# Kernel tuning notes

Hardware: AMD Instinct MI355X
Metric: run time of the kernel (lower is better)

## Reference

```python
import jax, jax.numpy as jnp
import numpy as np

K_STEPS = 10
ALPHA = 0.1
N_NODES = 100000
N_EDGES = 3200000

def setup_inputs() -> dict:
    key = jax.random.key(0)
    ks = jax.random.split(key, 6)
    x = jax.random.normal(ks[0], (N_NODES, 512), dtype=jnp.float32)
    edge_index = jax.random.randint(ks[1], (2, N_EDGES), 0, N_NODES, dtype=jnp.int64)
    W1 = jax.random.normal(ks[2], (512, 128), dtype=jnp.float32) * (1.0 / np.sqrt(512))
    b1 = jnp.zeros((128,), dtype=jnp.float32)
    W2 = jax.random.normal(ks[3], (128, 64), dtype=jnp.float32) * (1.0 / np.sqrt(128))
    b2 = jnp.zeros((64,), dtype=jnp.float32)
    return {"x": x, "edge_index": edge_index, "W1": W1, "b1": b1, "W2": W2, "b2": b2}

def _appnp_propagate(h, edge_index, n_nodes):
    # gcn_norm with self-loops: A_hat = D^-1/2 (A + I) D^-1/2
    self_loops = jnp.arange(n_nodes, dtype=edge_index.dtype)
    row = jnp.concatenate([edge_index[0], self_loops])  # source
    col = jnp.concatenate([edge_index[1], self_loops])  # target
    ew = jnp.ones(row.shape[0], dtype=h.dtype)
    deg = jax.ops.segment_sum(ew, col, num_segments=n_nodes)
    dis = jnp.where(deg > 0, jax.lax.rsqrt(deg), 0.0)
    norm = dis[row] * dis[col]  # [E+N]
    out = h
    for _ in range(K_STEPS):
        msg = norm[:, None] * out[row]                       # gather [E+N, C]
        agg = jax.ops.segment_sum(msg, col, num_segments=n_nodes)  # scatter
        out = (1.0 - ALPHA) * agg + ALPHA * h
    return out

def reference(x, edge_index, W1, b1, W2, b2):
    # eval mode: dropout is identity
    h = jax.nn.relu(x @ W1 + b1)
    h = h @ W2 + b2
    out = _appnp_propagate(h, edge_index, x.shape[0])
    return jax.nn.log_softmax(out, axis=1)
```

## Files before the change

kernel.cpp:

```cpp
#include <hip/hip_runtime.h>
#include <hip/hip_bf16.h>

#define N_NODES 100000
#define N_EDGES 3200000
#define C_OUT 64
#define C_HID 128
#define C_IN 512

typedef unsigned short u16;
typedef unsigned int u32;
using short8 = __attribute__((ext_vector_type(8))) short;
using f32x4 = __attribute__((ext_vector_type(4))) float;

__device__ __forceinline__ u32 f2bf(float f) {
    u32 x = __float_as_uint(f);
    return (x + 0x7fffu + ((x >> 16) & 1u)) >> 16;
}
__device__ __forceinline__ float bf2f_lo(u32 u) { return __uint_as_float(u << 16); }
__device__ __forceinline__ float bf2f_hi(u32 u) { return __uint_as_float(u & 0xffff0000u); }

__global__ __launch_bounds__(256) void hist_kernel(const int* __restrict__ cols,
                                                   int* __restrict__ cnt) {
    int e = blockIdx.x * 256 + threadIdx.x;
    if (e < N_EDGES) atomicAdd(&cnt[cols[e]], 1);
}

__global__ __launch_bounds__(256) void dis_kernel(const int* __restrict__ cnt,
                                                  float* __restrict__ dis) {
    int i = blockIdx.x * 256 + threadIdx.x;
    if (i < N_NODES) dis[i] = rsqrtf((float)(cnt[i] + 1));
}

__global__ __launch_bounds__(256) void scanA(const int* __restrict__ cnt,
                                             int* __restrict__ offs,
                                             int* __restrict__ bsum, int n) {
    __shared__ int sh[256];
    int b = blockIdx.x, tid = threadIdx.x;
    int base = b * 1024;
    int v[4]; int s = 0;
#pragma unroll
    for (int i = 0; i < 4; i++) {
        int idx = base + tid * 4 + i;
        v[i] = (idx < n) ? cnt[idx] : 0;
        s += v[i];
    }
    sh[tid] = s;
    __syncthreads();
    for (int st = 1; st < 256; st <<= 1) {
        int a = (tid >= st) ? sh[tid - st] : 0;
        int t = sh[tid];
        __syncthreads();
        sh[tid] = t + a;
        __syncthreads();
    }
    int run = sh[tid] - s;
#pragma unroll
    for (int i = 0; i < 4; i++) {
        int idx = base + tid * 4 + i;
        run += v[i];
        if (idx < n) offs[idx + 1] = run;
    }
    if (tid == 255) bsum[b] = sh[255];
}

__global__ __launch_bounds__(256) void scanB(int* __restrict__ bsum, int nb) {
    __shared__ int sh[256];
    int tid = threadIdx.x;
    int v = (tid < nb) ? bsum[tid] : 0;
    sh[tid] = v;
    __syncthreads();
    for (int st = 1; st < 256; st <<= 1) {
        int a = (tid >= st) ? sh[tid - st] : 0;
        int t = sh[tid];
        __syncthreads();
        sh[tid] = t + a;
        __syncthreads();
    }
    if (tid < nb) bsum[tid] = sh[tid] - v;
}

__global__ __launch_bounds__(256) void scanC(int* __restrict__ offs,
                                             const int* __restrict__ bsum, int n) {
    int idx = blockIdx.x * 256 + threadIdx.x;
    if (idx < n) offs[idx + 1] += bsum[idx >> 10];
    if (idx == 0) offs[0] = 0;
}

__global__ __launch_bounds__(256) void fill_kernel(const int* __restrict__ rows,
                                                   const int* __restrict__ cols,
                                                   const float* __restrict__ dis,
                                                   const int* __restrict__ offs,
                                                   int* __restrict__ cursor,
                                                   int* __restrict__ csr_row,
                                                   float* __restrict__ csr_norm) {
    int e = blockIdx.x * 256 + threadIdx.x;
    if (e >= N_EDGES) return;
    int r = rows[e], c = cols[e];
    float w = dis[r] * dis[c];
    int p = atomicAdd(&cursor[c], 1);
    int idx = offs[c] + p;
    csr_row[idx] = r;
    csr_norm[idx] = w;
}

__global__ __launch_bounds__(256) void w1t_kernel(const float* __restrict__ W1,
                                                  u16* __restrict__ W1T) {
    int idx = blockIdx.x * 256 + threadIdx.x;
    int n = idx >> 9, k = idx & 511;
    W1T[idx] = (u16)f2bf(W1[k * C_HID + n]);
}

__global__ __launch_bounds__(256) void gemm1_mfma(const float* __restrict__ X,
                                                  const u16* __restrict__ W1T,
                                                  const float* __restrict__ B1,
                                                  float* __restrict__ H1) {
    __shared__ u16 xs[64][56];
    __shared__ u16 wsT[128][56];
    int tid = threadIdx.x;
    int w = tid >> 6, l = tid & 63;
    int row0 = blockIdx.x * 64;

    f32x4 acc[8];
#pragma unroll
    for (int j = 0; j < 8; j++) acc[j] = (f32x4){0.f, 0.f, 0.f, 0.f};

    const int sr = tid >> 2;
    const int skq = (tid & 3) * 8;
    const int wn = tid >> 1;
    const int wkh = (tid & 1) * 16;

    for (int kb = 0; kb < C_IN; kb += 32) {
        {
            int gr = row0 + sr;
            float4 v0 = {0, 0, 0, 0}, v1 = {0, 0, 0, 0};
            if (gr < N_NODES) {
                const float4* px =
                    reinterpret_cast<const float4*>(X + (size_t)gr * C_IN + kb + skq);
                v0 = px[0];
                v1 = px[1];
            }
            uint4 pk;
            pk.x = f2bf(v0.x) | (f2bf(v0.y) << 16);
            pk.y = f2bf(v0.z) | (f2bf(v0.w) << 16);
            pk.z = f2bf(v1.x) | (f2bf(v1.y) << 16);
            pk.w = f2bf(v1.z) | (f2bf(v1.w) << 16);
            *reinterpret_cast<uint4*>(&xs[sr][skq]) = pk;
        }
        {
            const uint4* pw =
                reinterpret_cast<const uint4*>(W1T + (size_t)wn * C_IN + kb + wkh);
            *reinterpret_cast<uint4*>(&wsT[wn][wkh]) = pw[0];
            *reinterpret_cast<uint4*>(&wsT[wn][wkh + 8]) = pw[1];
        }
        __syncthreads();
        int ar = w * 16 + (l & 15);
        int koff = (l >> 4) * 8;
        short8 a = *reinterpret_cast<const short8*>(&xs[ar][koff]);
#pragma unroll
        for (int j = 0; j < 8; j++) {
            short8 b = *reinterpret_cast<const short8*>(&wsT[j * 16 + (l & 15)][koff]);
            acc[j] = __builtin_amdgcn_mfma_f32_16x16x32_bf16(a, b, acc[j], 0, 0, 0);
        }
        __syncthreads();
    }
    int col_lo = l & 15;
    int rbase = row0 + w * 16 + (l >> 4) * 4;
#pragma unroll
    for (int j = 0; j < 8; j++) {
        int col = j * 16 + col_lo;
        float bias = B1[col];
#pragma unroll
        for (int rr = 0; rr < 4; rr++) {
            int grow = rbase + rr;
            if (grow < N_NODES) {
                float v = acc[j][rr] + bias;
                H1[(size_t)grow * C_HID + col] = v > 0.f ? v : 0.f;
            }
        }
    }
}

__global__ __launch_bounds__(256) void gemm2(const float* __restrict__ H1,
                                             const float* __restrict__ W2,
                                             const float* __restrict__ B2,
                                             float* __restrict__ H) {
    __shared__ float hs[64][132];
    __shared__ float ws[128][64];
    int tid = threadIdx.x;
    int tx = tid & 15, ty = tid >> 4;
    int row0 = blockIdx.x * 64;
#pragma unroll
    for (int l = 0; l < 8; l++) {
        int idx = tid + l * 256;
        int k = idx >> 4;
        int c4 = idx & 15;
        *reinterpret_cast<float4*>(&ws[k][c4 * 4]) =
            *reinterpret_cast<const float4*>(W2 + (size_t)k * C_OUT + c4 * 4);
    }
#pragma unroll
    for (int l = 0; l < 8; l++) {
        int idx = tid + l * 256;
        int r = idx >> 5;
        int k4 = idx & 31;
        int gr = row0 + r;
        float4 v = {0, 0, 0, 0};
        if (gr < N_NODES)
            v = *reinterpret_cast<const float4*>(H1 + (size_t)gr * C_HID + k4 * 4);
        hs[r][k4 * 4 + 0] = v.x;
        hs[r][k4 * 4 + 1] = v.y;
        hs[r][k4 * 4 + 2] = v.z;
        hs[r][k4 * 4 + 3] = v.w;
    }
    __syncthreads();
    float acc[4][4];
#pragma unroll
    for (int i = 0; i < 4; i++)
#pragma unroll
        for (int j = 0; j < 4; j++) acc[i][j] = 0.f;
#pragma unroll 4
    for (int k = 0; k < C_HID; k++) {
        float hv[4], wv[4];
#pragma unroll
        for (int i = 0; i < 4; i++) hv[i] = hs[ty * 4 + i][k];
#pragma unroll
        for (int j = 0; j < 4; j++) wv[j] = ws[k][tx * 4 + j];
#pragma unroll
        for (int i = 0; i < 4; i++)
#pragma unroll
            for (int j = 0; j < 4; j++) acc[i][j] += hv[i] * wv[j];
    }
#pragma unroll
    for (int i = 0; i < 4; i++) {
        int gr = row0 + ty * 4 + i;
        if (gr < N_NODES) {
#pragma unroll
            for (int j = 0; j < 4; j++) {
                int c = tx * 4 + j;
                H[(size_t)gr * C_OUT + c] = acc[i][j] + B2[c];
            }
        }
    }
}

__global__ __launch_bounds__(256) void conv_bf16(const float* __restrict__ h,
                                                 u16* __restrict__ hb) {
    int idx = blockIdx.x * 256 + threadIdx.x;
    if (idx < N_NODES * 16) {
        float4 v = reinterpret_cast<const float4*>(h)[idx];
        uint2 o;
        o.x = f2bf(v.x) | (f2bf(v.y) << 16);
        o.y = f2bf(v.z) | (f2bf(v.w) << 16);
        reinterpret_cast<uint2*>(hb)[idx] = o;
    }
}

__global__ __launch_bounds__(256) void prop_bf16(const u16* __restrict__ src,
                                                 const float* __restrict__ hsrc,
                                                 u16* __restrict__ dst,
                                                 const int* __restrict__ offs,
                                                 const int* __restrict__ csr_row,
                                                 const float* __restrict__ csr_norm,
                                                 const float* __restrict__ dis) {
    int wid = (blockIdx.x * 256 + threadIdx.x) >> 6;
    if (wid >= N_NODES) return;
    int lane = threadIdx.x & 63;
    int g = lane >> 4;
    int cq = lane & 15;
    int beg = offs[wid], end = offs[wid + 1];
    float a0 = 0.f, a1 = 0.f, a2 = 0.f, a3 = 0.f;
    for (int j = beg; j < end; j += 4) {
        int jj = j + g;
        int r = 0;
        float w = 0.f;
        if (jj < end) {
            r = csr_row[jj];
            w = csr_norm[jj];
        }
        uint2 v = *reinterpret_cast<const uint2*>(src + ((size_t)r << 6) + (cq << 2));
        a0 += w * bf2f_lo(v.x);
        a1 += w * bf2f_hi(v.x);
        a2 += w * bf2f_lo(v.y);
        a3 += w * bf2f_hi(v.y);
    }
    a0 += __shfl_xor(a0, 16); a0 += __shfl_xor(a0, 32);
    a1 += __shfl_xor(a1, 16); a1 += __shfl_xor(a1, 32);
    a2 += __shfl_xor(a2, 16); a2 += __shfl_xor(a2, 32);
    a3 += __shfl_xor(a3, 16); a3 += __shfl_xor(a3, 32);
    if (g == 0) {
        float d = dis[wid];
        float d2 = d * d;
        size_t base = ((size_t)wid << 6) + (cq << 2);
        uint2 sv = *reinterpret_cast<const uint2*>(src + base);
        const float4 hv = *reinterpret_cast<const float4*>(hsrc + base);
        float o0 = 0.9f * (a0 + d2 * bf2f_lo(sv.x)) + 0.1f * hv.x;
        float o1 = 0.9f * (a1 + d2 * bf2f_hi(sv.x)) + 0.1f * hv.y;
        float o2 = 0.9f * (a2 + d2 * bf2f_lo(sv.y)) + 0.1f * hv.z;
        float o3 = 0.9f * (a3 + d2 * bf2f_hi(sv.y)) + 0.1f * hv.w;
        uint2 ov;
        ov.x = f2bf(o0) | (f2bf(o1) << 16);
        ov.y = f2bf(o2) | (f2bf(o3) << 16);
        *reinterpret_cast<uint2*>(dst + base) = ov;
    }
}

__global__ __launch_bounds__(256) void logsm_kernel(const u16* __restrict__ src,
                                                    float* __restrict__ out) {
    int wid = (blockIdx.x * 256 + threadIdx.x) >> 6;
    if (wid >= N_NODES) return;
    int lane = threadIdx.x & 63;
    float v = __uint_as_float(((u32)src[((size_t)wid << 6) + lane]) << 16);
    float m = v;
#pragma unroll
    for (int s = 1; s < 64; s <<= 1) m = fmaxf(m, __shfl_xor(m, s));
    float e = __expf(v - m);
    float sum = e;
#pragma unroll
    for (int s = 1; s < 64; s <<= 1) sum += __shfl_xor(sum, s);
    out[((size_t)wid << 6) + lane] = (v - m) - __logf(sum);
}

extern "C" void kernel_launch(void* const* d_in, const int* in_sizes, int n_in,
                              void* d_out, int out_size, void* d_ws, size_t ws_size,
                              hipStream_t stream) {
    const float* x = (const float*)d_in[0];
    const int* ei = (const int*)d_in[1];
    const float* W1 = (const float*)d_in[2];
    const float* B1 = (const float*)d_in[3];
    const float* W2 = (const float*)d_in[4];
    const float* B2 = (const float*)d_in[5];
    float* out = (float*)d_out;

    const int* rows = ei;
    const int* cols = ei + N_EDGES;

    char* p = (char*)d_ws;
    float* h1 = (float*)p;
    p += (size_t)N_NODES * C_HID * 4;
    float* h = (float*)p;
    p += (size_t)N_NODES * C_OUT * 4;
    int* csr_row = (int*)p;  p += (size_t)N_EDGES * 4;
    float* csr_norm = (float*)p; p += (size_t)N_EDGES * 4;
    int* cnt = (int*)p;      p += (size_t)N_NODES * 4;
    int* offs = (int*)p;     p += (size_t)(N_NODES + 1) * 4;
    int* cursor = (int*)p;   p += (size_t)N_NODES * 4;
    float* dis = (float*)p;  p += (size_t)N_NODES * 4;
    int* bsum = (int*)p;     p += 256 * 4;

    u16* W1T = (u16*)cursor;

    u16* hb = (u16*)h1;
    u16* stA = hb + (size_t)N_NODES * C_OUT;
    u16* stB = stA + (size_t)N_NODES * C_OUT;

    hipMemsetAsync(cnt, 0, (size_t)N_NODES * 4, stream);
    hipMemsetAsync(cursor, 0, (size_t)N_NODES * 4, stream);

    const int egrid = (N_EDGES + 255) / 256;
    const int ngrid = (N_NODES + 255) / 256;
    const int nscan = (N_NODES + 1023) / 1024;

    hist_kernel<<<egrid, 256, 0, stream>>>(cols, cnt);
    dis_kernel<<<ngrid, 256, 0, stream>>>(cnt, dis);
    scanA<<<nscan, 256, 0, stream>>>(cnt, offs, bsum, N_NODES);
    scanB<<<1, 256, 0, stream>>>(bsum, nscan);
    scanC<<<ngrid, 256, 0, stream>>>(offs, bsum, N_NODES);
    fill_kernel<<<egrid, 256, 0, stream>>>(rows, cols, dis, offs, cursor, csr_row, csr_norm);

    w1t_kernel<<<256, 256, 0, stream>>>(W1, W1T);

    const int mgrid = (N_NODES + 63) / 64;
    gemm1_mfma<<<mgrid, 256, 0, stream>>>(x, W1T, B1, h1 );
    gemm2<<<mgrid, 256, 0, stream>>>(h1, W2, B2, h);
    conv_bf16<<<(N_NODES * 16 + 255) / 256, 256, 0, stream>>>(h, hb);

    const int pgrid = N_NODES / 4;
    const u16* src = hb;
    u16* dst = stA;
    for (int k = 0; k < 10; k++) {
        prop_bf16<<<pgrid, 256, 0, stream>>>(src, h, dst, offs, csr_row, csr_norm, dis);
        src = dst;
        dst = (dst == stA) ? stB : stA;
    }
    logsm_kernel<<<pgrid, 256, 0, stream>>>(src, out);
}
```

Measured before the change: 1.727 ms.

## Pack CSR as int2 and widen propagation gathers to 16-byte loads

Interleaves the CSR source index and edge weight into a single 8-byte array so each edge needs one load. The propagation kernel is restructured to use 8 lanes per 64-channel row with 16-byte gathers, and processes 16 edges per iteration with two independent gathers per lane. Nontemporal loads are used for streaming edge data. This aims to raise memory-level parallelism and cut load instruction count in the gather-bound propagation, at the cost of more padding work for nodes whose degree is not a multiple of 16 and more registers.

New measurement: 1.388 ms. 19.7% less time.

```diff
diff --git a/kernel.cpp b/kernel.cpp
--- a/kernel.cpp
+++ b/kernel.cpp
@@ -9,6 +9,7 @@
 
 typedef unsigned short u16;
 typedef unsigned int u32;
+typedef long long ll;
 using short8 = __attribute__((ext_vector_type(8))) short;
 using f32x4 = __attribute__((ext_vector_type(4))) float;
 
@@ -22,7 +23,7 @@
 __global__ __launch_bounds__(256) void hist_kernel(const int* __restrict__ cols,
                                                    int* __restrict__ cnt) {
     int e = blockIdx.x * 256 + threadIdx.x;
-    if (e < N_EDGES) atomicAdd(&cnt[cols[e]], 1);
+    if (e < N_EDGES) atomicAdd(&cnt[__builtin_nontemporal_load(cols + e)], 1);
 }
 
 __global__ __launch_bounds__(256) void dis_kernel(const int* __restrict__ cnt,
@@ -91,16 +92,17 @@
                                                    const float* __restrict__ dis,
                                                    const int* __restrict__ offs,
                                                    int* __restrict__ cursor,
-                                                   int* __restrict__ csr_row,
-                                                   float* __restrict__ csr_norm) {
+                                                   int2* __restrict__ csr) {
     int e = blockIdx.x * 256 + threadIdx.x;
     if (e >= N_EDGES) return;
-    int r = rows[e], c = cols[e];
+    int r = __builtin_nontemporal_load(rows + e);
+    int c = __builtin_nontemporal_load(cols + e);
     float w = dis[r] * dis[c];
     int p = atomicAdd(&cursor[c], 1);
-    int idx = offs[c] + p;
-    csr_row[idx] = r;
-    csr_norm[idx] = w;
+    int2 val;
+    val.x = r;
+    val.y = __float_as_int(w);
+    csr[offs[c] + p] = val;
 }
 
 __global__ __launch_bounds__(256) void w1t_kernel(const float* __restrict__ W1,
@@ -258,48 +260,66 @@
                                                  const float* __restrict__ hsrc,
                                                  u16* __restrict__ dst,
                                                  const int* __restrict__ offs,
-                                                 const int* __restrict__ csr_row,
-                                                 const float* __restrict__ csr_norm,
+                                                 const ll* __restrict__ csr,
                                                  const float* __restrict__ dis) {
     int wid = (blockIdx.x * 256 + threadIdx.x) >> 6;
     if (wid >= N_NODES) return;
     int lane = threadIdx.x & 63;
-    int g = lane >> 4;
-    int cq = lane & 15;
+    int g = lane >> 3;
+    int c8 = lane & 7;
     int beg = offs[wid], end = offs[wid + 1];
     float a0 = 0.f, a1 = 0.f, a2 = 0.f, a3 = 0.f;
-    for (int j = beg; j < end; j += 4) {
-        int jj = j + g;
-        int r = 0;
-        float w = 0.f;
-        if (jj < end) {
-            r = csr_row[jj];
-            w = csr_norm[jj];
-        }
-        uint2 v = *reinterpret_cast<const uint2*>(src + ((size_t)r << 6) + (cq << 2));
-        a0 += w * bf2f_lo(v.x);
-        a1 += w * bf2f_hi(v.x);
-        a2 += w * bf2f_lo(v.y);
-        a3 += w * bf2f_hi(v.y);
-    }
-    a0 += __shfl_xor(a0, 16); a0 += __shfl_xor(a0, 32);
-    a1 += __shfl_xor(a1, 16); a1 += __shfl_xor(a1, 32);
-    a2 += __shfl_xor(a2, 16); a2 += __shfl_xor(a2, 32);
-    a3 += __shfl_xor(a3, 16); a3 += __shfl_xor(a3, 32);
+    float a4 = 0.f, a5 = 0.f, a6 = 0.f, a7 = 0.f;
+    const size_t coff = (size_t)(c8 << 3);
+    for (int j = beg; j < end; j += 16) {
+        int jj0 = j + g, jj1 = j + 8 + g;
+        ll e0 = 0, e1 = 0;
+        if (jj0 < end) e0 = __builtin_nontemporal_load(csr + jj0);
+        if (jj1 < end) e1 = __builtin_nontemporal_load(csr + jj1);
+        int r0 = (int)e0;
+        float w0 = __int_as_float((int)(e0 >> 32));
+        int r1 = (int)e1;
+        float w1 = __int_as_float((int)(e1 >> 32));
+        uint4 v0 = *reinterpret_cast<const uint4*>(src + (((size_t)r0) << 6) + coff);
+        uint4 v1 = *reinterpret_cast<const uint4*>(src + (((size_t)r1) << 6) + coff);
+        a0 += w0 * bf2f_lo(v0.x); a1 += w0 * bf2f_hi(v0.x);
+        a2 += w0 * bf2f_lo(v0.y); a3 += w0 * bf2f_hi(v0.y);
+        a4 += w0 * bf2f_lo(v0.z); a5 += w0 * bf2f_hi(v0.z);
+        a6 += w0 * bf2f_lo(v0.w); a7 += w0 * bf2f_hi(v0.w);
+        a0 += w1 * bf2f_lo(v1.x); a1 += w1 * bf2f_hi(v1.x);
+        a2 += w1 * bf2f_lo(v1.y); a3 += w1 * bf2f_hi(v1.y);
+        a4 += w1 * bf2f_lo(v1.z); a5 += w1 * bf2f_hi(v1.z);
+        a6 += w1 * bf2f_lo(v1.w); a7 += w1 * bf2f_hi(v1.w);
+    }
+    a0 += __shfl_xor(a0, 8); a0 += __shfl_xor(a0, 16); a0 += __shfl_xor(a0, 32);
+    a1 += __shfl_xor(a1, 8); a1 += __shfl_xor(a1, 16); a1 += __shfl_xor(a1, 32);
+    a2 += __shfl_xor(a2, 8); a2 += __shfl_xor(a2, 16); a2 += __shfl_xor(a2, 32);
+    a3 += __shfl_xor(a3, 8); a3 += __shfl_xor(a3, 16); a3 += __shfl_xor(a3, 32);
+    a4 += __shfl_xor(a4, 8); a4 += __shfl_xor(a4, 16); a4 += __shfl_xor(a4, 32);
+    a5 += __shfl_xor(a5, 8); a5 += __shfl_xor(a5, 16); a5 += __shfl_xor(a5, 32);
+    a6 += __shfl_xor(a6, 8); a6 += __shfl_xor(a6, 16); a6 += __shfl_xor(a6, 32);
+    a7 += __shfl_xor(a7, 8); a7 += __shfl_xor(a7, 16); a7 += __shfl_xor(a7, 32);
     if (g == 0) {
         float d = dis[wid];
         float d2 = d * d;
-        size_t base = ((size_t)wid << 6) + (cq << 2);
-        uint2 sv = *reinterpret_cast<const uint2*>(src + base);
-        const float4 hv = *reinterpret_cast<const float4*>(hsrc + base);
-        float o0 = 0.9f * (a0 + d2 * bf2f_lo(sv.x)) + 0.1f * hv.x;
-        float o1 = 0.9f * (a1 + d2 * bf2f_hi(sv.x)) + 0.1f * hv.y;
-        float o2 = 0.9f * (a2 + d2 * bf2f_lo(sv.y)) + 0.1f * hv.z;
-        float o3 = 0.9f * (a3 + d2 * bf2f_hi(sv.y)) + 0.1f * hv.w;
-        uint2 ov;
+        size_t base = ((size_t)wid << 6) + coff;
+        uint4 sv = *reinterpret_cast<const uint4*>(src + base);
+        const float4* hp = reinterpret_cast<const float4*>(hsrc + base);
+        float4 h0 = hp[0], h1v = hp[1];
+        float o0 = 0.9f * (a0 + d2 * bf2f_lo(sv.x)) + 0.1f * h0.x;
+        float o1 = 0.9f * (a1 + d2 * bf2f_hi(sv.x)) + 0.1f * h0.y;
+        float o2 = 0.9f * (a2 + d2 * bf2f_lo(sv.y)) + 0.1f * h0.z;
+        float o3 = 0.9f * (a3 + d2 * bf2f_hi(sv.y)) + 0.1f * h0.w;
+        float o4 = 0.9f * (a4 + d2 * bf2f_lo(sv.z)) + 0.1f * h1v.x;
+        float o5 = 0.9f * (a5 + d2 * bf2f_hi(sv.z)) + 0.1f * h1v.y;
+        float o6 = 0.9f * (a6 + d2 * bf2f_lo(sv.w)) + 0.1f * h1v.z;
+        float o7 = 0.9f * (a7 + d2 * bf2f_hi(sv.w)) + 0.1f * h1v.w;
+        uint4 ov;
         ov.x = f2bf(o0) | (f2bf(o1) << 16);
         ov.y = f2bf(o2) | (f2bf(o3) << 16);
-        *reinterpret_cast<uint2*>(dst + base) = ov;
+        ov.z = f2bf(o4) | (f2bf(o5) << 16);
+        ov.w = f2bf(o6) | (f2bf(o7) << 16);
+        *reinterpret_cast<uint4*>(dst + base) = ov;
     }
 }
 
@@ -338,8 +358,7 @@
     p += (size_t)N_NODES * C_HID * 4;
     float* h = (float*)p;
     p += (size_t)N_NODES * C_OUT * 4;
-    int* csr_row = (int*)p;  p += (size_t)N_EDGES * 4;
-    float* csr_norm = (float*)p; p += (size_t)N_EDGES * 4;
+    int2* csr = (int2*)p; p += (size_t)N_EDGES * 8;
     int* cnt = (int*)p;      p += (size_t)N_NODES * 4;
     int* offs = (int*)p;     p += (size_t)(N_NODES + 1) * 4;
     int* cursor = (int*)p;   p += (size_t)N_NODES * 4;
@@ -364,12 +383,12 @@
     scanA<<<nscan, 256, 0, stream>>>(cnt, offs, bsum, N_NODES);
     scanB<<<1, 256, 0, stream>>>(bsum, nscan);
     scanC<<<ngrid, 256, 0, stream>>>(offs, bsum, N_NODES);
-    fill_kernel<<<egrid, 256, 0, stream>>>(rows, cols, dis, offs, cursor, csr_row, csr_norm);
+    fill_kernel<<<egrid, 256, 0, stream>>>(rows, cols, dis, offs, cursor, csr);
 
     w1t_kernel<<<256, 256, 0, stream>>>(W1, W1T);
 
     const int mgrid = (N_NODES + 63) / 64;
-    gemm1_mfma<<<mgrid, 256, 0, stream>>>(x, W1T, B1, h1 );
+    gemm1_mfma<<<mgrid, 256, 0, stream>>>(x, W1T, B1, h1);
     gemm2<<<mgrid, 256, 0, stream>>>(h1, W2, B2, h);
     conv_bf16<<<(N_NODES * 16 + 255) / 256, 256, 0, stream>>>(h, hb);
 
@@ -377,7 +396,7 @@
     const u16* src = hb;
     u16* dst = stA;
     for (int k = 0; k < 10; k++) {
-        prop_bf16<<<pgrid, 256, 0, stream>>>(src, h, dst, offs, csr_row, csr_norm, dis);
+        prop_bf16<<<pgrid, 256, 0, stream>>>(src, h, dst, offs, (const ll*)csr, dis);
         src = dst;
         dst = (dst == stA) ? stB : stA;
     }
```
